# Optimization experiments

Hardware: AMD Instinct MI355X
Metric: run time of the kernel (lower is better)

Reference implementation:

```python
import jax, jax.numpy as jnp
import numpy as np

HID = 1024
VOCAB = 32000


def setup_inputs() -> dict:
    key = jax.random.key(0)
    ks = jax.random.split(key, 10)
    B, T, S, H, V = 64, 128, 128, HID, VOCAB
    s = 1.0 / np.sqrt(H)
    inp = {
        "tgt": jax.random.randint(ks[0], (B, T), 0, V),
        "h0": jax.random.normal(ks[1], (1, B, H), dtype=jnp.float32),
        "c0": jax.random.normal(ks[2], (1, B, H), dtype=jnp.float32),
        "encoder_outputs": jax.random.normal(ks[3], (B, S, H), dtype=jnp.float32),
        "src_lengths": jax.random.randint(ks[4], (B,), 1, S + 1),
        "emb_table": jax.random.normal(ks[5], (V, H), dtype=jnp.float32),
        "w_ih": jax.random.uniform(ks[6], (4 * H, H), minval=-s, maxval=s, dtype=jnp.float32),
        "w_hh": jax.random.uniform(ks[7], (4 * H, H), minval=-s, maxval=s, dtype=jnp.float32),
        "b_ih": jax.random.uniform(ks[8], (4 * H,), minval=-s, maxval=s, dtype=jnp.float32),
        "b_hh": jax.random.uniform(ks[9], (4 * H,), minval=-s, maxval=s, dtype=jnp.float32),
    }
    return inp


def _lstm_scan(xs, h0, c0, w_ih, w_hh, b_ih, b_hh):
    # xs: [T', B, H]; PyTorch gate order i, f, g, o
    def step(carry, x):
        h, c = carry
        gates = x @ w_ih.T + b_ih + h @ w_hh.T + b_hh  # [B, 4H]
        i, f, g, o = jnp.split(gates, 4, axis=-1)
        c = jax.nn.sigmoid(f) * c + jax.nn.sigmoid(i) * jnp.tanh(g)
        h = jax.nn.sigmoid(o) * jnp.tanh(c)
        return (h, c), h

    (h, c), ys = jax.lax.scan(step, (h0, c0), xs)
    return ys, h, c


def reference(tgt, h0, c0, encoder_outputs, src_lengths, emb_table, w_ih, w_hh, b_ih, b_hh):
    # padding_idx=0: that embedding row is pinned to zero
    emb_table = emb_table.at[0].set(0.0)
    embedded = emb_table[tgt]  # [B, T, H]; dropout(p=0) = identity
    T = tgt.shape[1]
    n_steps = T - 1 if T > 1 else 1  # torch loop feeds inputs 0..T-2
    xs = jnp.transpose(embedded[:, :n_steps, :], (1, 0, 2))  # [T', B, H]
    ys, h, c = _lstm_scan(xs, h0[0], c0[0], w_ih, w_hh, b_ih, b_hh)
    outputs = jnp.transpose(ys, (1, 0, 2))  # [B, T', H]; attn=None, dropout=identity
    return outputs, h[None], c[None]
```

## Files before the change

### kernel.cpp

```cpp
#include <hip/hip_runtime.h>
#include <cstdint>
#include <cstddef>

#define HID   1024
#define G4    4096
#define BB    64
#define TSEQ  128
#define NSTEP 127
#define AGT   __HIP_MEMORY_SCOPE_AGENT

typedef __attribute__((ext_vector_type(4))) float f32x4;
typedef __attribute__((ext_vector_type(8))) short bf16x8;

__device__ __forceinline__ unsigned short f2bf(float x) {
  union { float f; unsigned u; } v; v.f = x;
  unsigned r = v.u + 0x7FFF + ((v.u >> 16) & 1);
  return (unsigned short)(r >> 16);
}
__device__ __forceinline__ float fsigm(float x) { return 1.0f / (1.0f + __expf(-x)); }
__device__ __forceinline__ float ftanh(float x) { return 2.0f / (1.0f + __expf(-2.0f * x)) - 1.0f; }

__global__ __launch_bounds__(256) void conv_f32_bf16(
    const float* __restrict__ in, unsigned short* __restrict__ out, int n)
{
  int i = (blockIdx.x * 256 + threadIdx.x) * 8;
  if (i >= n) return;
  float4 v0 = *reinterpret_cast<const float4*>(&in[i]);
  float4 v1 = *reinterpret_cast<const float4*>(&in[i + 4]);
  unsigned short u[8];
  u[0] = f2bf(v0.x); u[1] = f2bf(v0.y); u[2] = f2bf(v0.z); u[3] = f2bf(v0.w);
  u[4] = f2bf(v1.x); u[5] = f2bf(v1.y); u[6] = f2bf(v1.z); u[7] = f2bf(v1.w);
  *reinterpret_cast<bf16x8*>(&out[i]) = *reinterpret_cast<bf16x8*>(u);
}

__global__ __launch_bounds__(256) void bias_add(
    const float* __restrict__ b_ih, const float* __restrict__ b_hh,
    float* __restrict__ bias)
{
  int i = blockIdx.x * 256 + threadIdx.x;
  if (i < G4) bias[i] = b_ih[i] + b_hh[i];
}

__global__ __launch_bounds__(256) void conv_A(
    const int* __restrict__ tgt, const float* __restrict__ emb,
    unsigned short* __restrict__ A, int t0, int tc)
{
  int i = blockIdx.x * 256 + threadIdx.x;
  int m  = i >> 7;
  int k8 = (i & 127) * 8;
  int tl = m >> 6, b = m & 63;
  float4 v0 = make_float4(0.f, 0.f, 0.f, 0.f), v1 = v0;
  if (tl < tc) {
    int tok = tgt[b * TSEQ + t0 + tl];
    if (tok != 0) {
      const float* src = &emb[(size_t)tok * HID + k8];
      v0 = *reinterpret_cast<const float4*>(src);
      v1 = *reinterpret_cast<const float4*>(src + 4);
    }
  }
  unsigned short u[8];
  u[0] = f2bf(v0.x); u[1] = f2bf(v0.y); u[2] = f2bf(v0.z); u[3] = f2bf(v0.w);
  u[4] = f2bf(v1.x); u[5] = f2bf(v1.y); u[6] = f2bf(v1.z); u[7] = f2bf(v1.w);
  *reinterpret_cast<bf16x8*>(&A[(size_t)m * HID + k8]) = *reinterpret_cast<bf16x8*>(u);
}

__global__ __launch_bounds__(256, 1) void lstm_persist(
    const unsigned short* __restrict__ whh, const unsigned short* __restrict__ wih,
    const unsigned short* __restrict__ xbf, const float* __restrict__ bias,
    unsigned int* __restrict__ hb0, unsigned int* __restrict__ hb1,
    float* __restrict__ c_ws, const float* __restrict__ c0,
    float* __restrict__ out, unsigned int* __restrict__ flags,
    int t0, int tc)
{
  __shared__ unsigned short wi_lds[4 * 4 * 8 * 512];
  __shared__ float red[4][4][16][16];

  const int tid = threadIdx.x;
  const int l = tid & 63, w = tid >> 6;
  const int lr = l & 15, lh = l >> 4;
  const int grp = blockIdx.x >> 6;
  const int ub  = blockIdx.x & 63;
  const int b0 = grp * 16;
  const int u0 = ub * 16;

  for (int idx = tid; idx < 8192; idx += 256) {
    int ll = idx & 63, kk = (idx >> 6) & 7, g = (idx >> 9) & 3, ww = (idx >> 11) & 3;
    bf16x8 v = *reinterpret_cast<const bf16x8*>(
        &wih[(size_t)(g * HID + u0 + (ll & 15)) * HID + ww * 256 + kk * 32 + (ll >> 4) * 8]);
    *reinterpret_cast<bf16x8*>(&wi_lds[(size_t)idx * 8]) = v;
  }

  const int bi = tid >> 4, ui = tid & 15;
  const size_t ci = (size_t)(b0 + bi) * HID + u0 + ui;
  float c_reg = (t0 == 0) ? c0[ci] : c_ws[ci];

  float bias_r[4];
#pragma unroll
  for (int g = 0; g < 4; ++g) bias_r[g] = bias[g * HID + u0 + ui];

  __syncthreads();

  const size_t hbase = ((size_t)(b0 + lr) * HID) >> 1;

  for (int tl = 0; tl < tc; ++tl) {
    const int t = t0 + tl;
    const unsigned int* hin  = (t & 1) ? hb1 : hb0;
    unsigned int*       hout = (t & 1) ? hb0 : hb1;

    bf16x8 bw[4][8];
#pragma unroll
    for (int g = 0; g < 4; ++g)
#pragma unroll
      for (int kk = 0; kk < 8; ++kk)
        bw[g][kk] = *reinterpret_cast<const bf16x8*>(
            &whh[(size_t)(g * HID + u0 + lr) * HID + w * 256 + kk * 32 + lh * 8]);

    f32x4 acc[4];
#pragma unroll
    for (int g = 0; g < 4; ++g) acc[g] = (f32x4)0.f;
#pragma unroll
    for (int kk = 0; kk < 8; ++kk) {
      bf16x8 ax = *reinterpret_cast<const bf16x8*>(
          &xbf[((size_t)tl * BB + b0 + lr) * HID + w * 256 + kk * 32 + lh * 8]);
#pragma unroll
      for (int g = 0; g < 4; ++g) {
        bf16x8 bi2 = *reinterpret_cast<const bf16x8*>(
            &wi_lds[(size_t)(((w * 4 + g) * 8 + kk) * 512 + l * 8)]);
        acc[g] = __builtin_amdgcn_mfma_f32_16x16x32_bf16(ax, bi2, acc[g], 0, 0, 0);
      }
    }

    if (t > 0) {
      const unsigned int* fl = flags + (((size_t)(t - 1) * 4 + grp) * 64 + l) * 4;
      while (true) {
        unsigned v = __hip_atomic_load(fl, __ATOMIC_RELAXED, AGT);
        if (__all(v != 0)) break;
        __builtin_amdgcn_s_sleep(2);
      }
    }

#pragma unroll
    for (int kk = 0; kk < 8; ++kk) {
      size_t base = hbase + (size_t)w * 128 + kk * 16 + lh * 4;
      unsigned long long lo = __hip_atomic_load(
          reinterpret_cast<const unsigned long long*>(&hin[base]), __ATOMIC_RELAXED, AGT);
      unsigned long long hi = __hip_atomic_load(
          reinterpret_cast<const unsigned long long*>(&hin[base + 2]), __ATOMIC_RELAXED, AGT);
      union { unsigned long long q[2]; bf16x8 v; } u;
      u.q[0] = lo; u.q[1] = hi;
      bf16x8 af = u.v;
#pragma unroll
      for (int g = 0; g < 4; ++g)
        acc[g] = __builtin_amdgcn_mfma_f32_16x16x32_bf16(af, bw[g][kk], acc[g], 0, 0, 0);
    }

#pragma unroll
    for (int g = 0; g < 4; ++g)
#pragma unroll
      for (int r = 0; r < 4; ++r)
        red[w][g][lh * 4 + r][lr] = acc[g][r];
    __syncthreads();

    float gates[4];
#pragma unroll
    for (int g = 0; g < 4; ++g)
      gates[g] = red[0][g][bi][ui] + red[1][g][bi][ui] +
                 red[2][g][bi][ui] + red[3][g][bi][ui] + bias_r[g];

    float iv = fsigm(gates[0]);
    float fv = fsigm(gates[1]);
    float gv = ftanh(gates[2]);
    float ov = fsigm(gates[3]);
    c_reg = fv * c_reg + iv * gv;
    float hn = ov * ftanh(c_reg);

    unsigned hv = (unsigned)f2bf(hn);
    unsigned pv = (unsigned)__shfl_xor((int)hv, 1);
    if ((tid & 1) == 0) {
      unsigned word = (hv & 0xffffu) | (pv << 16);
      __hip_atomic_store(&hout[ci >> 1], word, __ATOMIC_RELAXED, AGT);
    }

    asm volatile("s_waitcnt vmcnt(0)");
    __syncthreads();
    if (tid == 0)
      __hip_atomic_store(&flags[(((size_t)t * 4 + grp) * 64 + ub) * 4], 1u,
                         __ATOMIC_RELAXED, AGT);

    out[((size_t)(b0 + bi) * NSTEP + t) * HID + u0 + ui] = hn;
    if (t == NSTEP - 1) {
      size_t tail = (size_t)BB * NSTEP * HID;
      out[tail + ci] = hn;
      out[tail + (size_t)BB * HID + ci] = c_reg;
    }
  }
  c_ws[ci] = c_reg;
}

extern "C" void kernel_launch(void* const* d_in, const int* in_sizes, int n_in,
                              void* d_out, int out_size, void* d_ws, size_t ws_size,
                              hipStream_t stream)
{
  const int*   tgt  = (const int*)d_in[0];
  const float* h0   = (const float*)d_in[1];
  const float* c0   = (const float*)d_in[2];
  const float* emb  = (const float*)d_in[5];
  const float* w_ih = (const float*)d_in[6];
  const float* w_hh = (const float*)d_in[7];
  const float* b_ih = (const float*)d_in[8];
  const float* b_hh = (const float*)d_in[9];
  float* out = (float*)d_out;

  const size_t FLAGS_BYTES = (size_t)NSTEP * 4 * 64 * 16;

  char* p = (char*)d_ws;
  unsigned short* wih_bf = (unsigned short*)p;  p += (size_t)G4 * HID * 2;
  unsigned short* whh_bf = (unsigned short*)p;  p += (size_t)G4 * HID * 2;
  float*          bias   = (float*)p;           p += (size_t)G4 * 4;
  unsigned int*   hb0    = (unsigned int*)p;    p += (size_t)BB * HID * 2;
  unsigned int*   hb1    = (unsigned int*)p;    p += (size_t)BB * HID * 2;
  float*          c_ws   = (float*)p;           p += (size_t)BB * HID * 4;
  unsigned int*   flags  = (unsigned int*)p;    p += FLAGS_BYTES;

  size_t fixed = (size_t)(p - (char*)d_ws);
  size_t rem = (ws_size > fixed) ? ws_size - fixed : 0;
  int Tc = (int)(rem / ((size_t)BB * HID * 2));
  if (Tc > NSTEP) Tc = NSTEP;
  if (Tc < 1) return;
  unsigned short* x_bf = (unsigned short*)p;

  hipMemsetAsync(flags, 0, FLAGS_BYTES, stream);
  conv_f32_bf16<<<dim3((G4 * HID) / 8 / 256), 256, 0, stream>>>(w_ih, wih_bf, G4 * HID);
  conv_f32_bf16<<<dim3((G4 * HID) / 8 / 256), 256, 0, stream>>>(w_hh, whh_bf, G4 * HID);
  bias_add<<<dim3(G4 / 256), 256, 0, stream>>>(b_ih, b_hh, bias);
  conv_f32_bf16<<<dim3((BB * HID) / 8 / 256), 256, 0, stream>>>(h0, (unsigned short*)hb0, BB * HID);

  for (int t0 = 0; t0 < NSTEP; t0 += Tc) {
    int tc = (NSTEP - t0 < Tc) ? (NSTEP - t0) : Tc;
    conv_A<<<dim3(tc * 32), 256, 0, stream>>>(tgt, emb, x_bf, t0, tc);

    void* kargs[] = { (void*)&whh_bf, (void*)&wih_bf, (void*)&x_bf, (void*)&bias,
                      (void*)&hb0, (void*)&hb1, (void*)&c_ws, (void*)&c0,
                      (void*)&out, (void*)&flags, (void*)&t0, (void*)&tc };
    hipLaunchCooperativeKernel((void*)lstm_persist, dim3(256), dim3(256),
                               kargs, 0, stream);
  }
}
```

Baseline: 668.8 us.

## Keep recurrent weights in LDS and precompute next step's input projection before waiting

The W_hh slice now sits in LDS and the W_ih slice is streamed from global memory, instead of the reverse. Loading recurrent weights from LDS shortens the critical path after the flag wait. The input-projection MFMAs for the next timestep are issued at the end of the current step, so they overlap the time other blocks spend finishing. The flag spin-sleep is also shortened. In exchange, W_ih is re-read from global or L2 every step, and the extra vmcnt(0) wait may serialize those loads.

```diff
diff --git a/kernel.cpp b/kernel.cpp
--- a/kernel.cpp
+++ b/kernel.cpp
@@ -72,7 +72,7 @@
     float* __restrict__ out, unsigned int* __restrict__ flags,
     int t0, int tc)
 {
-  __shared__ unsigned short wi_lds[4 * 4 * 8 * 512];
+  __shared__ unsigned short wh_lds[4 * 4 * 8 * 512];
   __shared__ float red[4][4][16][16];
 
   const int tid = threadIdx.x;
@@ -86,8 +86,8 @@
   for (int idx = tid; idx < 8192; idx += 256) {
     int ll = idx & 63, kk = (idx >> 6) & 7, g = (idx >> 9) & 3, ww = (idx >> 11) & 3;
     bf16x8 v = *reinterpret_cast<const bf16x8*>(
-        &wih[(size_t)(g * HID + u0 + (ll & 15)) * HID + ww * 256 + kk * 32 + (ll >> 4) * 8]);
-    *reinterpret_cast<bf16x8*>(&wi_lds[(size_t)idx * 8]) = v;
+        &whh[(size_t)(g * HID + u0 + (ll & 15)) * HID + ww * 256 + kk * 32 + (ll >> 4) * 8]);
+    *reinterpret_cast<bf16x8*>(&wh_lds[(size_t)idx * 8]) = v;
   }
 
   const int bi = tid >> 4, ui = tid & 15;
@@ -101,41 +101,33 @@
   __syncthreads();
 
   const size_t hbase = ((size_t)(b0 + lr) * HID) >> 1;
+
+  f32x4 acc[4];
+#pragma unroll
+  for (int g = 0; g < 4; ++g) acc[g] = (f32x4)0.f;
+#pragma unroll
+  for (int kk = 0; kk < 8; ++kk) {
+    bf16x8 ax = *reinterpret_cast<const bf16x8*>(
+        &xbf[((size_t)0 * BB + b0 + lr) * HID + w * 256 + kk * 32 + lh * 8]);
+#pragma unroll
+    for (int g = 0; g < 4; ++g) {
+      bf16x8 bw = *reinterpret_cast<const bf16x8*>(
+          &wih[(size_t)(g * HID + u0 + lr) * HID + w * 256 + kk * 32 + lh * 8]);
+      acc[g] = __builtin_amdgcn_mfma_f32_16x16x32_bf16(ax, bw, acc[g], 0, 0, 0);
+    }
+  }
 
   for (int tl = 0; tl < tc; ++tl) {
     const int t = t0 + tl;
     const unsigned int* hin  = (t & 1) ? hb1 : hb0;
     unsigned int*       hout = (t & 1) ? hb0 : hb1;
-
-    bf16x8 bw[4][8];
-#pragma unroll
-    for (int g = 0; g < 4; ++g)
-#pragma unroll
-      for (int kk = 0; kk < 8; ++kk)
-        bw[g][kk] = *reinterpret_cast<const bf16x8*>(
-            &whh[(size_t)(g * HID + u0 + lr) * HID + w * 256 + kk * 32 + lh * 8]);
-
-    f32x4 acc[4];
-#pragma unroll
-    for (int g = 0; g < 4; ++g) acc[g] = (f32x4)0.f;
-#pragma unroll
-    for (int kk = 0; kk < 8; ++kk) {
-      bf16x8 ax = *reinterpret_cast<const bf16x8*>(
-          &xbf[((size_t)tl * BB + b0 + lr) * HID + w * 256 + kk * 32 + lh * 8]);
-#pragma unroll
-      for (int g = 0; g < 4; ++g) {
-        bf16x8 bi2 = *reinterpret_cast<const bf16x8*>(
-            &wi_lds[(size_t)(((w * 4 + g) * 8 + kk) * 512 + l * 8)]);
-        acc[g] = __builtin_amdgcn_mfma_f32_16x16x32_bf16(ax, bi2, acc[g], 0, 0, 0);
-      }
-    }
 
     if (t > 0) {
       const unsigned int* fl = flags + (((size_t)(t - 1) * 4 + grp) * 64 + l) * 4;
       while (true) {
         unsigned v = __hip_atomic_load(fl, __ATOMIC_RELAXED, AGT);
         if (__all(v != 0)) break;
-        __builtin_amdgcn_s_sleep(2);
+        __builtin_amdgcn_s_sleep(1);
       }
     }
 
@@ -150,8 +142,11 @@
       u.q[0] = lo; u.q[1] = hi;
       bf16x8 af = u.v;
 #pragma unroll
-      for (int g = 0; g < 4; ++g)
-        acc[g] = __builtin_amdgcn_mfma_f32_16x16x32_bf16(af, bw[g][kk], acc[g], 0, 0, 0);
+      for (int g = 0; g < 4; ++g) {
+        bf16x8 bw = *reinterpret_cast<const bf16x8*>(
+            &wh_lds[(size_t)(((w * 4 + g) * 8 + kk) * 512 + l * 8)]);
+        acc[g] = __builtin_amdgcn_mfma_f32_16x16x32_bf16(af, bw, acc[g], 0, 0, 0);
+      }
     }
 
 #pragma unroll
@@ -180,7 +175,6 @@
       unsigned word = (hv & 0xffffu) | (pv << 16);
       __hip_atomic_store(&hout[ci >> 1], word, __ATOMIC_RELAXED, AGT);
     }
-
     asm volatile("s_waitcnt vmcnt(0)");
     __syncthreads();
     if (tid == 0)
@@ -193,6 +187,23 @@
       out[tail + ci] = hn;
       out[tail + (size_t)BB * HID + ci] = c_reg;
     }
+
+#pragma unroll
+    for (int g = 0; g < 4; ++g) acc[g] = (f32x4)0.f;
+    if (tl + 1 < tc) {
+#pragma unroll
+      for (int kk = 0; kk < 8; ++kk) {
+        bf16x8 ax = *reinterpret_cast<const bf16x8*>(
+            &xbf[((size_t)(tl + 1) * BB + b0 + lr) * HID + w * 256 + kk * 32 + lh * 8]);
+#pragma unroll
+        for (int g = 0; g < 4; ++g) {
+          bf16x8 bw = *reinterpret_cast<const bf16x8*>(
+              &wih[(size_t)(g * HID + u0 + lr) * HID + w * 256 + kk * 32 + lh * 8]);
+          acc[g] = __builtin_amdgcn_mfma_f32_16x16x32_bf16(ax, bw, acc[g], 0, 0, 0);
+        }
+      }
+    }
+    asm volatile("s_waitcnt vmcnt(0)");
   }
   c_ws[ci] = c_reg;
 }
```

New measurement: 1.083 ms. 61.9% more time.
